# Performance work log

Hardware: AMD Instinct MI355X
Metric: run time of the kernel (lower is better)

The kernel has to match this reference:

```python
import jax, jax.numpy as jnp
import numpy as np
import math

B, S, E, H = 2, 2048, 1024, 16
Dh = E // H

def setup_inputs() -> dict:
    key = jax.random.key(0)
    ks = jax.random.split(key, 11)
    s_in = 1.0 / math.sqrt(E)
    return {
        "key": jax.random.normal(ks[0], (B, S, E), jnp.float32),
        "query": jax.random.normal(ks[1], (B, S, E), jnp.float32),
        "value": jax.random.normal(ks[2], (B, S, E), jnp.float32),
        "Wq": jax.random.normal(ks[3], (E, E), jnp.float32) * s_in,
        "bq": jnp.zeros((E,), jnp.float32),
        "Wk": jax.random.normal(ks[4], (E, E), jnp.float32) * s_in,
        "bk": jnp.zeros((E,), jnp.float32),
        "Wv": jax.random.normal(ks[5], (E, E), jnp.float32) * s_in,
        "bv": jnp.zeros((E,), jnp.float32),
        "Wo": jax.random.normal(ks[6], (E, E), jnp.float32) * s_in,
        "bo": jnp.zeros((E,), jnp.float32),
    }

def _split_heads(x):
    # [B,S,E] -> [B,H,S,Dh]
    b, s, _ = x.shape
    return x.reshape(b, s, H, Dh).transpose(0, 2, 1, 3)

def reference(key, query, value, Wq, bq, Wk, bk, Wv, bv, Wo, bo):
    k = _split_heads(key @ Wk.T + bk)
    q = _split_heads(query @ Wq.T + bq)
    v = _split_heads(value @ Wv.T + bv)
    scale = 1.0 / math.sqrt(Dh)
    # [B,H,S,S] score matrix (faithful to naive implementation)
    scores = jnp.einsum("bhqd,bhkd->bhqk", q, k) * scale
    probs = jax.nn.softmax(scores, axis=-1)
    attn = jnp.einsum("bhqk,bhkd->bhqd", probs, v)  # [B,H,S,Dh]
    out = attn.transpose(0, 2, 1, 3).reshape(key.shape[0], key.shape[1], E)
    return out @ Wo.T + bo
```

## Files before the change

### kernel.cpp

```cpp
#include <hip/hip_runtime.h>
#include <hip/hip_bf16.h>
#include <stdint.h>

typedef short    bf16x8 __attribute__((ext_vector_type(8)));
typedef float    f32x4  __attribute__((ext_vector_type(4)));
typedef float    f32x16 __attribute__((ext_vector_type(16)));
typedef uint32_t u32x2  __attribute__((ext_vector_type(2)));
typedef uint32_t u32x4  __attribute__((ext_vector_type(4)));
typedef uint16_t u16x4  __attribute__((ext_vector_type(4)));

#define DEV __device__ __forceinline__
#define AS1 __attribute__((address_space(1)))
#define AS3 __attribute__((address_space(3)))

DEV uint32_t pk_bf16(float lo, float hi) {
    uint32_t r;
    asm("v_cvt_pk_bf16_f32 %0, %1, %2" : "=v"(r) : "v"(lo), "v"(hi));
    return r;
}

DEV void gload_lds16(const uint16_t* g, uint16_t* l) {
    __builtin_amdgcn_global_load_lds((AS1 const uint32_t*)g, (AS3 uint32_t*)l, 16, 0, 0);
}

__global__ __launch_bounds__(256) void cast_all(
    const float* __restrict__ w0, const float* __restrict__ w1,
    const float* __restrict__ w2, const float* __restrict__ w3,
    const float* __restrict__ aq, const float* __restrict__ ak, const float* __restrict__ av,
    uint16_t* __restrict__ ws)
{
    const int y = blockIdx.y;
    const float* s;
    uint16_t* d;
    if (y < 4) {
        if (blockIdx.x >= 512) return;
        s = (y == 0) ? w0 : (y == 1) ? w1 : (y == 2) ? w2 : w3;
        d = ws + ((size_t)y << 20);
    } else {
        s = (y == 4) ? aq : (y == 5) ? ak : av;
        d = ws + (size_t)(1 << 22) + ((size_t)(y - 4) << 22);
    }
    const size_t i = ((size_t)blockIdx.x * 256 + threadIdx.x) * 8;
    float4 a = *reinterpret_cast<const float4*>(s + i);
    float4 b = *reinterpret_cast<const float4*>(s + i + 4);
    u32x4 w;
    w[0] = pk_bf16(a.x, a.y); w[1] = pk_bf16(a.z, a.w);
    w[2] = pk_bf16(b.x, b.y); w[3] = pk_bf16(b.z, b.w);
    *reinterpret_cast<u32x4*>(d + i) = w;
}

__global__ __launch_bounds__(256) void gemm_qkv(
    const uint16_t* __restrict__ Qc, const uint16_t* __restrict__ Kc, const uint16_t* __restrict__ Vc,
    const uint16_t* __restrict__ wqc, const uint16_t* __restrict__ wkc, const uint16_t* __restrict__ wvc,
    const float* __restrict__ bq, const float* __restrict__ bk, const float* __restrict__ bv,
    uint16_t* __restrict__ Qb, uint16_t* __restrict__ Kb, uint16_t* __restrict__ Vt)
{
    constexpr int Kd = 1024, N = 1024;
    __shared__ uint16_t Al[128 * 32];
    __shared__ uint16_t Bl[128 * 32];

    const int z = blockIdx.z;
    const uint16_t* A = (z == 0) ? Qc : (z == 1) ? Kc : Vc;
    const uint16_t* W = (z == 0) ? wqc : (z == 1) ? wkc : wvc;
    const float* bias = (z == 0) ? bq : (z == 1) ? bk : bv;

    const int brow = blockIdx.x * 128;
    const int bcol = blockIdx.y * 128;
    const int t = threadIdx.x, lane = t & 63, wid = t >> 6;
    const int wr = wid >> 1, wc = wid & 1;

    const int srow = wid * 16 + (lane >> 2);
    const int scol = (lane & 3) * 8;
    const uint16_t* aA = A + (size_t)(brow + srow) * Kd + scol;
    const uint16_t* aW = W + (size_t)(bcol + srow) * Kd + scol;
    uint16_t* lA = &Al[srow * 32 + scol];
    uint16_t* lB = &Bl[srow * 32 + scol];

    f32x4 acc[4][4];
#pragma unroll
    for (int i = 0; i < 4; ++i)
#pragma unroll
        for (int j = 0; j < 4; ++j)
#pragma unroll
            for (int e = 0; e < 4; ++e) acc[i][j][e] = 0.f;

    const int frow = lane & 15;
    const int koff = (lane >> 4) * 8;

    for (int k0 = 0; k0 < Kd; k0 += 32) {
        gload_lds16(aA + k0, lA);
        gload_lds16(aA + k0 + (size_t)64 * Kd, lA + 64 * 32);
        gload_lds16(aW + k0, lB);
        gload_lds16(aW + k0 + (size_t)64 * Kd, lB + 64 * 32);
        __syncthreads();

        bf16x8 af[4], bfr[4];
#pragma unroll
        for (int fr = 0; fr < 4; ++fr)
            af[fr] = *reinterpret_cast<const bf16x8*>(&Al[(wr * 64 + fr * 16 + frow) * 32 + koff]);
#pragma unroll
        for (int fc = 0; fc < 4; ++fc)
            bfr[fc] = *reinterpret_cast<const bf16x8*>(&Bl[(wc * 64 + fc * 16 + frow) * 32 + koff]);
#pragma unroll
        for (int fr = 0; fr < 4; ++fr)
#pragma unroll
            for (int fc = 0; fc < 4; ++fc)
                acc[fr][fc] = __builtin_amdgcn_mfma_f32_16x16x32_bf16(af[fr], bfr[fc], acc[fr][fc], 0, 0, 0);
        __syncthreads();
    }

    const int m0 = brow + wr * 64;
    const int n0 = bcol + wc * 64;
    if (z < 2) {
        uint16_t* Cb = (z == 0) ? Qb : Kb;
#pragma unroll
        for (int fc = 0; fc < 4; ++fc) {
            const int col = n0 + fc * 16 + frow;
            const float bia = bias[col];
#pragma unroll
            for (int fr = 0; fr < 4; ++fr) {
                const int mrow = m0 + fr * 16 + (lane >> 4) * 4;
                f32x4 a = acc[fr][fc];
                uint32_t w01 = pk_bf16(a[0] + bia, a[1] + bia);
                uint32_t w23 = pk_bf16(a[2] + bia, a[3] + bia);
                Cb[(size_t)(mrow + 0) * N + col] = (uint16_t)(w01 & 0xffff);
                Cb[(size_t)(mrow + 1) * N + col] = (uint16_t)(w01 >> 16);
                Cb[(size_t)(mrow + 2) * N + col] = (uint16_t)(w23 & 0xffff);
                Cb[(size_t)(mrow + 3) * N + col] = (uint16_t)(w23 >> 16);
            }
        }
    } else {
#pragma unroll
        for (int fc = 0; fc < 4; ++fc) {
            const int col = n0 + fc * 16 + frow;
            const int hh = col >> 6, dd = col & 63;
            const float bia = bias[col];
#pragma unroll
            for (int fr = 0; fr < 4; ++fr) {
                const int mrow = m0 + fr * 16 + (lane >> 4) * 4;
                const int bb = mrow >> 11, ss = mrow & 2047;
                f32x4 a = acc[fr][fc];
                uint32_t w01 = pk_bf16(a[0] + bia, a[1] + bia);
                uint32_t w23 = pk_bf16(a[2] + bia, a[3] + bia);
                u16x4 pv;
                pv[0] = (uint16_t)(w01 & 0xffff); pv[1] = (uint16_t)(w01 >> 16);
                pv[2] = (uint16_t)(w23 & 0xffff); pv[3] = (uint16_t)(w23 >> 16);
                *reinterpret_cast<u16x4*>(&Vt[(size_t)((bb * 16 + hh) * 64 + dd) * 2048 + ss]) = pv;
            }
        }
    }
}

__global__ __launch_bounds__(256) void attn_kernel(
    const uint16_t* __restrict__ Qb, const uint16_t* __restrict__ Kb,
    const uint16_t* __restrict__ Vt, uint16_t* __restrict__ At)
{
    constexpr int S = 2048, E = 1024;
    __shared__ uint16_t Kl[64 * 72];
    __shared__ uint16_t Vl[64 * 72];

    const int bh = blockIdx.y;
    const int b = bh >> 4, h = bh & 15;
    const int t = threadIdx.x;
    const int lane = t & 63, wid = t >> 6;
    const int lo = lane & 31, hi = lane >> 5;
    const int q0 = blockIdx.x * 128 + wid * 32;

    bf16x8 qf[4];
    {
        const uint16_t* qrow = Qb + (size_t)(b * S + q0 + lo) * E + h * 64;
#pragma unroll
        for (int kk = 0; kk < 4; ++kk)
            qf[kk] = *reinterpret_cast<const bf16x8*>(qrow + kk * 16 + hi * 8);
    }

    f32x16 oacc[2];
#pragma unroll
    for (int i = 0; i < 16; ++i) { oacc[0][i] = 0.f; oacc[1][i] = 0.f; }
    float mrun = -1e30f, lsum = 0.f;
    const float cexp = 0.18033688011112042f;

    const uint16_t* Kbase = Kb + (size_t)(b * S) * E + h * 64;
    const uint16_t* Vbase = Vt + (size_t)(bh * 64) * S;

    for (int kv0 = 0; kv0 < S; kv0 += 64) {
        {
            const int r = t >> 2, seg = t & 3;
            const uint16_t* ks = Kbase + (size_t)(kv0 + r) * E + seg * 16;
            u32x4 k0 = *reinterpret_cast<const u32x4*>(ks);
            u32x4 k1 = *reinterpret_cast<const u32x4*>(ks + 8);
            const uint16_t* vs = Vbase + (size_t)r * S + kv0 + seg * 16;
            u32x4 v0 = *reinterpret_cast<const u32x4*>(vs);
            u32x4 v1 = *reinterpret_cast<const u32x4*>(vs + 8);
            *reinterpret_cast<u32x4*>(&Kl[r * 72 + seg * 16])     = k0;
            *reinterpret_cast<u32x4*>(&Kl[r * 72 + seg * 16 + 8]) = k1;
            *reinterpret_cast<u32x4*>(&Vl[r * 72 + seg * 16])     = v0;
            *reinterpret_cast<u32x4*>(&Vl[r * 72 + seg * 16 + 8]) = v1;
        }
        __syncthreads();

        f32x16 sacc[2];
#pragma unroll
        for (int i = 0; i < 16; ++i) { sacc[0][i] = 0.f; sacc[1][i] = 0.f; }
#pragma unroll
        for (int kk = 0; kk < 4; ++kk) {
            bf16x8 ka0 = *reinterpret_cast<const bf16x8*>(&Kl[lo * 72 + kk * 16 + hi * 8]);
            bf16x8 ka1 = *reinterpret_cast<const bf16x8*>(&Kl[(32 + lo) * 72 + kk * 16 + hi * 8]);
            sacc[0] = __builtin_amdgcn_mfma_f32_32x32x16_bf16(ka0, qf[kk], sacc[0], 0, 0, 0);
            sacc[1] = __builtin_amdgcn_mfma_f32_32x32x16_bf16(ka1, qf[kk], sacc[1], 0, 0, 0);
        }

        float pmax = sacc[0][0];
#pragma unroll
        for (int r = 1; r < 16; ++r) pmax = fmaxf(pmax, sacc[0][r]);
#pragma unroll
        for (int r = 0; r < 16; ++r) pmax = fmaxf(pmax, sacc[1][r]);
        pmax = fmaxf(pmax, __shfl_xor(pmax, 32, 64));

        if (__any(pmax > mrun)) {
            float mnew = fmaxf(mrun, pmax);
            float corr = __builtin_amdgcn_exp2f((mrun - mnew) * cexp);
            lsum *= corr;
#pragma unroll
            for (int i = 0; i < 16; ++i) { oacc[0][i] *= corr; oacc[1][i] *= corr; }
            mrun = mnew;
        }

        uint32_t w[16];
        float psum = 0.f;
#pragma unroll
        for (int kf = 0; kf < 2; ++kf)
#pragma unroll
            for (int j = 0; j < 8; ++j) {
                float pa = __builtin_amdgcn_exp2f((sacc[kf][2 * j]     - mrun) * cexp);
                float pb = __builtin_amdgcn_exp2f((sacc[kf][2 * j + 1] - mrun) * cexp);
                psum += pa + pb;
                w[kf * 8 + j] = pk_bf16(pa, pb);
            }
        lsum += psum + __shfl_xor(psum, 32, 64);

        uint32_t x[16];
#pragma unroll
        for (int i = 0; i < 16; ++i) x[i] = __shfl_xor(w[i], 32, 64);

#pragma unroll
        for (int ks = 0; ks < 4; ++ks) {
            const int base = (ks >> 1) * 8 + (ks & 1) * 4;
            u32x4 pw;
            if (hi == 0) {
                pw[0] = w[base + 0]; pw[1] = w[base + 1];
                pw[2] = x[base + 0]; pw[3] = x[base + 1];
            } else {
                pw[0] = x[base + 2]; pw[1] = x[base + 3];
                pw[2] = w[base + 2]; pw[3] = w[base + 3];
            }
            bf16x8 pf = __builtin_bit_cast(bf16x8, pw);
#pragma unroll
            for (int df = 0; df < 2; ++df) {
                bf16x8 vf = *reinterpret_cast<const bf16x8*>(&Vl[(df * 32 + lo) * 72 + ks * 16 + hi * 8]);
                oacc[df] = __builtin_amdgcn_mfma_f32_32x32x16_bf16(vf, pf, oacc[df], 0, 0, 0);
            }
        }
        __syncthreads();
    }

    const float inv = 1.0f / lsum;
    uint16_t* orow = At + (size_t)(b * S + q0 + lo) * E + h * 64;
#pragma unroll
    for (int df = 0; df < 2; ++df)
#pragma unroll
        for (int g = 0; g < 4; ++g) {
            uint32_t w01 = pk_bf16(oacc[df][4 * g + 0] * inv, oacc[df][4 * g + 1] * inv);
            uint32_t w23 = pk_bf16(oacc[df][4 * g + 2] * inv, oacc[df][4 * g + 3] * inv);
            u32x2 o2; o2[0] = w01; o2[1] = w23;
            *reinterpret_cast<u32x2*>(orow + df * 32 + 8 * g + 4 * hi) = o2;
        }
}

__global__ __launch_bounds__(256) void gemm_out(
    const uint16_t* __restrict__ Atn, const uint16_t* __restrict__ woc,
    const float* __restrict__ bo, float* __restrict__ out)
{
    constexpr int Kd = 1024, N = 1024;
    __shared__ uint16_t Al[128 * 32];
    __shared__ uint16_t Bl[128 * 32];

    const int brow = blockIdx.x * 128;
    const int bcol = blockIdx.y * 128;
    const int t = threadIdx.x, lane = t & 63, wid = t >> 6;
    const int wr = wid >> 1, wc = wid & 1;

    const int srow = wid * 16 + (lane >> 2);
    const int scol = (lane & 3) * 8;
    const uint16_t* aA = Atn + (size_t)(brow + srow) * Kd + scol;
    const uint16_t* aW = woc + (size_t)(bcol + srow) * Kd + scol;
    uint16_t* lA = &Al[srow * 32 + scol];
    uint16_t* lB = &Bl[srow * 32 + scol];

    f32x4 acc[4][4];
#pragma unroll
    for (int i = 0; i < 4; ++i)
#pragma unroll
        for (int j = 0; j < 4; ++j)
#pragma unroll
            for (int e = 0; e < 4; ++e) acc[i][j][e] = 0.f;

    const int frow = lane & 15;
    const int koff = (lane >> 4) * 8;

    for (int k0 = 0; k0 < Kd; k0 += 32) {
        gload_lds16(aA + k0, lA);
        gload_lds16(aA + k0 + (size_t)64 * Kd, lA + 64 * 32);
        gload_lds16(aW + k0, lB);
        gload_lds16(aW + k0 + (size_t)64 * Kd, lB + 64 * 32);
        __syncthreads();

        bf16x8 af[4], bfr[4];
#pragma unroll
        for (int fr = 0; fr < 4; ++fr)
            af[fr] = *reinterpret_cast<const bf16x8*>(&Al[(wr * 64 + fr * 16 + frow) * 32 + koff]);
#pragma unroll
        for (int fc = 0; fc < 4; ++fc)
            bfr[fc] = *reinterpret_cast<const bf16x8*>(&Bl[(wc * 64 + fc * 16 + frow) * 32 + koff]);
#pragma unroll
        for (int fr = 0; fr < 4; ++fr)
#pragma unroll
            for (int fc = 0; fc < 4; ++fc)
                acc[fr][fc] = __builtin_amdgcn_mfma_f32_16x16x32_bf16(af[fr], bfr[fc], acc[fr][fc], 0, 0, 0);
        __syncthreads();
    }

    const int m0 = brow + wr * 64;
    const int n0 = bcol + wc * 64;
#pragma unroll
    for (int fc = 0; fc < 4; ++fc) {
        const int col = n0 + fc * 16 + frow;
        const float bia = bo[col];
#pragma unroll
        for (int fr = 0; fr < 4; ++fr) {
            const int mrow = m0 + fr * 16 + (lane >> 4) * 4;
#pragma unroll
            for (int j = 0; j < 4; ++j)
                out[(size_t)(mrow + j) * N + col] = acc[fr][fc][j] + bia;
        }
    }
}

extern "C" void kernel_launch(void* const* d_in, const int* in_sizes, int n_in,
                              void* d_out, int out_size, void* d_ws, size_t ws_size,
                              hipStream_t stream)
{
    const float* key   = (const float*)d_in[0];
    const float* query = (const float*)d_in[1];
    const float* value = (const float*)d_in[2];
    const float* Wq = (const float*)d_in[3];
    const float* bq = (const float*)d_in[4];
    const float* Wk = (const float*)d_in[5];
    const float* bk = (const float*)d_in[6];
    const float* Wv = (const float*)d_in[7];
    const float* bv = (const float*)d_in[8];
    const float* Wo = (const float*)d_in[9];
    const float* bo = (const float*)d_in[10];

    uint16_t* ws = (uint16_t*)d_ws;
    uint16_t* wqc = ws;
    uint16_t* wkc = ws + ((size_t)1 << 20);
    uint16_t* wvc = ws + ((size_t)2 << 20);
    uint16_t* woc = ws + ((size_t)3 << 20);
    uint16_t* Qc  = ws + ((size_t)1 << 22);
    uint16_t* Kc  = ws + ((size_t)2 << 22);
    uint16_t* Vc  = ws + ((size_t)3 << 22);
    uint16_t* Qb  = ws + ((size_t)4 << 22);
    uint16_t* Kb  = ws + ((size_t)5 << 22);
    uint16_t* Vt  = ws + ((size_t)6 << 22);
    uint16_t* At  = Qc;
    float* out = (float*)d_out;

    cast_all<<<dim3(2048, 7), 256, 0, stream>>>(Wq, Wk, Wv, Wo, query, key, value, ws);
    gemm_qkv<<<dim3(32, 8, 3), 256, 0, stream>>>(Qc, Kc, Vc, wqc, wkc, wvc,
                                                 bq, bk, bv, Qb, Kb, Vt);
    attn_kernel<<<dim3(16, 32), 256, 0, stream>>>(Qb, Kb, Vt, At);
    gemm_out<<<dim3(32, 8), 256, 0, stream>>>(At, woc, bo, out);
}
```

Baseline: 157.8 us.

## Double-buffer K/V tiles in attention and fold softmax scale into Q weights

The attention loop now prefetches the next K/V tile into registers while computing the current one, then writes it to a second LDS buffer, so each tile needs one barrier instead of two. The softmax scale (log2e/sqrt(Dh)) is folded into the Wq cast and the q bias, which removes the multiply before each exp2. The kernel also rescales the running output only when the tile max exceeds the running max by more than 3, raises wave priority around the MFMA blocks, and splits the max and sum reductions into trees. The trade-off is more LDS and register pressure, plus slightly larger bf16 rounding from pre-scaling Q.

```diff
diff --git a/kernel.cpp b/kernel.cpp
--- a/kernel.cpp
+++ b/kernel.cpp
@@ -12,6 +12,8 @@
 #define DEV __device__ __forceinline__
 #define AS1 __attribute__((address_space(1)))
 #define AS3 __attribute__((address_space(3)))
+
+#define SM_SCALE 0.18033688011112042f
 
 DEV uint32_t pk_bf16(float lo, float hi) {
     uint32_t r;
@@ -40,12 +42,13 @@
         s = (y == 4) ? aq : (y == 5) ? ak : av;
         d = ws + (size_t)(1 << 22) + ((size_t)(y - 4) << 22);
     }
+    const float m = (y == 0) ? SM_SCALE : 1.0f;
     const size_t i = ((size_t)blockIdx.x * 256 + threadIdx.x) * 8;
     float4 a = *reinterpret_cast<const float4*>(s + i);
     float4 b = *reinterpret_cast<const float4*>(s + i + 4);
     u32x4 w;
-    w[0] = pk_bf16(a.x, a.y); w[1] = pk_bf16(a.z, a.w);
-    w[2] = pk_bf16(b.x, b.y); w[3] = pk_bf16(b.z, b.w);
+    w[0] = pk_bf16(a.x * m, a.y * m); w[1] = pk_bf16(a.z * m, a.w * m);
+    w[2] = pk_bf16(b.x * m, b.y * m); w[3] = pk_bf16(b.z * m, b.w * m);
     *reinterpret_cast<u32x4*>(d + i) = w;
 }
 
@@ -63,6 +66,7 @@
     const uint16_t* A = (z == 0) ? Qc : (z == 1) ? Kc : Vc;
     const uint16_t* W = (z == 0) ? wqc : (z == 1) ? wkc : wvc;
     const float* bias = (z == 0) ? bq : (z == 1) ? bk : bv;
+    const float bs = (z == 0) ? SM_SCALE : 1.0f;
 
     const int brow = blockIdx.x * 128;
     const int bcol = blockIdx.y * 128;
@@ -116,7 +120,7 @@
 #pragma unroll
         for (int fc = 0; fc < 4; ++fc) {
             const int col = n0 + fc * 16 + frow;
-            const float bia = bias[col];
+            const float bia = bias[col] * bs;
 #pragma unroll
             for (int fr = 0; fr < 4; ++fr) {
                 const int mrow = m0 + fr * 16 + (lane >> 4) * 4;
@@ -156,8 +160,8 @@
     const uint16_t* __restrict__ Vt, uint16_t* __restrict__ At)
 {
     constexpr int S = 2048, E = 1024;
-    __shared__ uint16_t Kl[64 * 72];
-    __shared__ uint16_t Vl[64 * 72];
+    __shared__ uint16_t Kl[2][64 * 72];
+    __shared__ uint16_t Vl[2][64 * 72];
 
     const int bh = blockIdx.y;
     const int b = bh >> 4, h = bh & 15;
@@ -178,48 +182,66 @@
 #pragma unroll
     for (int i = 0; i < 16; ++i) { oacc[0][i] = 0.f; oacc[1][i] = 0.f; }
     float mrun = -1e30f, lsum = 0.f;
-    const float cexp = 0.18033688011112042f;
 
     const uint16_t* Kbase = Kb + (size_t)(b * S) * E + h * 64;
     const uint16_t* Vbase = Vt + (size_t)(bh * 64) * S;
 
-    for (int kv0 = 0; kv0 < S; kv0 += 64) {
-        {
-            const int r = t >> 2, seg = t & 3;
-            const uint16_t* ks = Kbase + (size_t)(kv0 + r) * E + seg * 16;
-            u32x4 k0 = *reinterpret_cast<const u32x4*>(ks);
-            u32x4 k1 = *reinterpret_cast<const u32x4*>(ks + 8);
-            const uint16_t* vs = Vbase + (size_t)r * S + kv0 + seg * 16;
-            u32x4 v0 = *reinterpret_cast<const u32x4*>(vs);
-            u32x4 v1 = *reinterpret_cast<const u32x4*>(vs + 8);
-            *reinterpret_cast<u32x4*>(&Kl[r * 72 + seg * 16])     = k0;
-            *reinterpret_cast<u32x4*>(&Kl[r * 72 + seg * 16 + 8]) = k1;
-            *reinterpret_cast<u32x4*>(&Vl[r * 72 + seg * 16])     = v0;
-            *reinterpret_cast<u32x4*>(&Vl[r * 72 + seg * 16 + 8]) = v1;
-        }
-        __syncthreads();
+    const int r = t >> 2, seg = t & 3;
+
+    {
+        const uint16_t* ks = Kbase + (size_t)r * E + seg * 16;
+        const uint16_t* vs = Vbase + (size_t)r * S + seg * 16;
+        u32x4 k0 = *reinterpret_cast<const u32x4*>(ks);
+        u32x4 k1 = *reinterpret_cast<const u32x4*>(ks + 8);
+        u32x4 v0 = *reinterpret_cast<const u32x4*>(vs);
+        u32x4 v1 = *reinterpret_cast<const u32x4*>(vs + 8);
+        *reinterpret_cast<u32x4*>(&Kl[0][r * 72 + seg * 16])     = k0;
+        *reinterpret_cast<u32x4*>(&Kl[0][r * 72 + seg * 16 + 8]) = k1;
+        *reinterpret_cast<u32x4*>(&Vl[0][r * 72 + seg * 16])     = v0;
+        *reinterpret_cast<u32x4*>(&Vl[0][r * 72 + seg * 16 + 8]) = v1;
+        __syncthreads();
+    }
+
+    auto tile = [&](const uint16_t* Klb, const uint16_t* Vlb,
+                    uint16_t* Kn, uint16_t* Vn, int kv0) {
+        const bool more = (kv0 + 64) < S;
+        u32x4 nk0, nk1, nv0, nv1;
+        if (more) {
+            const uint16_t* ks = Kbase + (size_t)(kv0 + 64 + r) * E + seg * 16;
+            const uint16_t* vs = Vbase + (size_t)r * S + (kv0 + 64) + seg * 16;
+            nk0 = *reinterpret_cast<const u32x4*>(ks);
+            nk1 = *reinterpret_cast<const u32x4*>(ks + 8);
+            nv0 = *reinterpret_cast<const u32x4*>(vs);
+            nv1 = *reinterpret_cast<const u32x4*>(vs + 8);
+        }
 
         f32x16 sacc[2];
 #pragma unroll
         for (int i = 0; i < 16; ++i) { sacc[0][i] = 0.f; sacc[1][i] = 0.f; }
+        __builtin_amdgcn_s_setprio(1);
 #pragma unroll
         for (int kk = 0; kk < 4; ++kk) {
-            bf16x8 ka0 = *reinterpret_cast<const bf16x8*>(&Kl[lo * 72 + kk * 16 + hi * 8]);
-            bf16x8 ka1 = *reinterpret_cast<const bf16x8*>(&Kl[(32 + lo) * 72 + kk * 16 + hi * 8]);
+            bf16x8 ka0 = *reinterpret_cast<const bf16x8*>(&Klb[lo * 72 + kk * 16 + hi * 8]);
+            bf16x8 ka1 = *reinterpret_cast<const bf16x8*>(&Klb[(32 + lo) * 72 + kk * 16 + hi * 8]);
             sacc[0] = __builtin_amdgcn_mfma_f32_32x32x16_bf16(ka0, qf[kk], sacc[0], 0, 0, 0);
             sacc[1] = __builtin_amdgcn_mfma_f32_32x32x16_bf16(ka1, qf[kk], sacc[1], 0, 0, 0);
         }
-
-        float pmax = sacc[0][0];
-#pragma unroll
-        for (int r = 1; r < 16; ++r) pmax = fmaxf(pmax, sacc[0][r]);
-#pragma unroll
-        for (int r = 0; r < 16; ++r) pmax = fmaxf(pmax, sacc[1][r]);
+        __builtin_amdgcn_s_setprio(0);
+
+        float tm[16];
+#pragma unroll
+        for (int i = 0; i < 16; ++i) tm[i] = fmaxf(sacc[0][i], sacc[1][i]);
+#pragma unroll
+        for (int s = 8; s > 0; s >>= 1)
+#pragma unroll
+            for (int i = 0; i < 8; ++i)
+                if (i < s) tm[i] = fmaxf(tm[i], tm[i + s]);
+        float pmax = tm[0];
         pmax = fmaxf(pmax, __shfl_xor(pmax, 32, 64));
 
-        if (__any(pmax > mrun)) {
+        if (!__all(pmax - mrun <= 3.0f)) {
             float mnew = fmaxf(mrun, pmax);
-            float corr = __builtin_amdgcn_exp2f((mrun - mnew) * cexp);
+            float corr = __builtin_amdgcn_exp2f(mrun - mnew);
             lsum *= corr;
 #pragma unroll
             for (int i = 0; i < 16; ++i) { oacc[0][i] *= corr; oacc[1][i] *= corr; }
@@ -227,22 +249,24 @@
         }
 
         uint32_t w[16];
-        float psum = 0.f;
+        float ps0 = 0.f, ps1 = 0.f, ps2 = 0.f, ps3 = 0.f;
 #pragma unroll
         for (int kf = 0; kf < 2; ++kf)
 #pragma unroll
             for (int j = 0; j < 8; ++j) {
-                float pa = __builtin_amdgcn_exp2f((sacc[kf][2 * j]     - mrun) * cexp);
-                float pb = __builtin_amdgcn_exp2f((sacc[kf][2 * j + 1] - mrun) * cexp);
-                psum += pa + pb;
+                float pa = __builtin_amdgcn_exp2f(sacc[kf][2 * j]     - mrun);
+                float pb = __builtin_amdgcn_exp2f(sacc[kf][2 * j + 1] - mrun);
+                if (j & 1) { ps0 += pa; ps1 += pb; } else { ps2 += pa; ps3 += pb; }
                 w[kf * 8 + j] = pk_bf16(pa, pb);
             }
+        float psum = (ps0 + ps1) + (ps2 + ps3);
         lsum += psum + __shfl_xor(psum, 32, 64);
 
         uint32_t x[16];
 #pragma unroll
         for (int i = 0; i < 16; ++i) x[i] = __shfl_xor(w[i], 32, 64);
 
+        __builtin_amdgcn_s_setprio(1);
 #pragma unroll
         for (int ks = 0; ks < 4; ++ks) {
             const int base = (ks >> 1) * 8 + (ks & 1) * 4;
@@ -257,11 +281,24 @@
             bf16x8 pf = __builtin_bit_cast(bf16x8, pw);
 #pragma unroll
             for (int df = 0; df < 2; ++df) {
-                bf16x8 vf = *reinterpret_cast<const bf16x8*>(&Vl[(df * 32 + lo) * 72 + ks * 16 + hi * 8]);
+                bf16x8 vf = *reinterpret_cast<const bf16x8*>(&Vlb[(df * 32 + lo) * 72 + ks * 16 + hi * 8]);
                 oacc[df] = __builtin_amdgcn_mfma_f32_32x32x16_bf16(vf, pf, oacc[df], 0, 0, 0);
             }
         }
-        __syncthreads();
+        __builtin_amdgcn_s_setprio(0);
+
+        if (more) {
+            *reinterpret_cast<u32x4*>(&Kn[r * 72 + seg * 16])     = nk0;
+            *reinterpret_cast<u32x4*>(&Kn[r * 72 + seg * 16 + 8]) = nk1;
+            *reinterpret_cast<u32x4*>(&Vn[r * 72 + seg * 16])     = nv0;
+            *reinterpret_cast<u32x4*>(&Vn[r * 72 + seg * 16 + 8]) = nv1;
+        }
+        __syncthreads();
+    };
+
+    for (int kv0 = 0; kv0 < S; kv0 += 128) {
+        tile(Kl[0], Vl[0], Kl[1], Vl[1], kv0);
+        tile(Kl[1], Vl[1], Kl[0], Vl[0], kv0 + 64);
     }
 
     const float inv = 1.0f / lsum;
```

New measurement: 142.9 us. 1.1x faster.
